# Optimization experiments

Measured on AMD Instinct MI355X. Metric: run time of the kernel, lower is better.

Reference implementation:

```python
import jax, jax.numpy as jnp
import numpy as np

DECAY_MIN = 0.9
DECAY_MAX = 0.999

def setup_inputs() -> dict:
    key = jax.random.key(0)
    ks = jax.random.split(key, 6)
    B, L, D, M = 8, 4096, 1024, 64
    s = 0.02
    return {
        "x": jax.random.normal(ks[0], (B, L, D), jnp.float32),
        "Wq": jax.random.normal(ks[1], (D, M), jnp.float32) * s,
        "Wk": jax.random.normal(ks[2], (D, M), jnp.float32) * s,
        "Wv": jax.random.normal(ks[3], (D, M), jnp.float32) * s,
        "Wo": jax.random.normal(ks[4], (M, D), jnp.float32) * s,
        "bo": jnp.zeros((D,), jnp.float32),
        "Wg": jax.random.normal(ks[5], (D, 1), jnp.float32) * s,
        "bg": jnp.zeros((1,), jnp.float32),
        "decay_param": jnp.full((1,), 0.5, jnp.float32),
    }

def reference(x, Wq, Wk, Wv, Wo, bo, Wg, bg, decay_param):
    B, L, D = x.shape
    M = Wq.shape[1]
    # decay in [DECAY_MIN, DECAY_MAX], shape (1,) -> scalar broadcast
    decay = DECAY_MIN + jax.nn.sigmoid(decay_param) * (DECAY_MAX - DECAY_MIN)
    q = x @ Wq  # (B,L,M)
    k = x @ Wk
    v = x @ Wv
    gates = jax.nn.sigmoid(x @ Wg + bg)[..., 0]  # (B,L)
    S0 = jnp.zeros((B, M, M), x.dtype)

    def scan_fn(S, inp):
        q_t, k_t, v_t, g_t = inp  # (B,M),(B,M),(B,M),(B,)
        gk = k_t * g_t[:, None]
        gv = v_t * g_t[:, None]
        # fast-weight update: S = decay*S + gk ⊗ gv
        S = decay * S + gk[:, :, None] * gv[:, None, :]
        out_t = jnp.einsum('bd,bde->be', q_t, S)
        return S, out_t

    S_final, outs = jax.lax.scan(
        scan_fn, S0,
        (q.transpose(1, 0, 2), k.transpose(1, 0, 2), v.transpose(1, 0, 2), gates.T))
    outs = outs.transpose(1, 0, 2)  # (B,L,M)
    y = outs @ Wo + bo  # (B,L,D); dropout deterministic (eval)
    return y, S_final
```

## Files before the change

kernel.cpp:

```cpp
#include <hip/hip_runtime.h>
#include <math.h>

#define B_SZ 8
#define L_SZ 4096
#define D_SZ 1024
#define M_SZ 64
#define ROWS (B_SZ * L_SZ)
#define NCHUNK 64
#define CHUNK 64

#define FMA4(acc, sc, v) { (acc).x += (sc)*(v).x; (acc).y += (sc)*(v).y; (acc).z += (sc)*(v).z; (acc).w += (sc)*(v).w; }
#define SCALE4(v, sc) { (v).x *= (sc); (v).y *= (sc); (v).z *= (sc); (v).w *= (sc); }

typedef __attribute__((ext_vector_type(8))) short bf16x8;
typedef __attribute__((ext_vector_type(4))) float f32x4;

__device__ __forceinline__ float sigmoid_f(float z) { return 1.0f / (1.0f + __expf(-z)); }
__device__ __forceinline__ float decay_of(const float* __restrict__ dp) {
  return 0.9f + (0.999f - 0.9f) * sigmoid_f(dp[0]);
}
__device__ __forceinline__ unsigned short f2bf(float f) {
  unsigned int u = __float_as_uint(f);
  unsigned int r = (u + 0x7FFFu + ((u >> 16) & 1u)) >> 16;
  return (unsigned short)r;
}

__device__ __forceinline__ void gl2lds16(const void* g, void* l) {
  __builtin_amdgcn_global_load_lds(
      (const __attribute__((address_space(1))) unsigned int*)g,
      (__attribute__((address_space(3))) unsigned int*)l, 16, 0, 0);
}

#define BT_CH     1872
#define BT_CH_PAD 1920
#define BT_BYTES  (BT_CH_PAD * 16)
__global__ __launch_bounds__(256) void k0_prep(
    const float* __restrict__ Wq, const float* __restrict__ Wk,
    const float* __restrict__ Wv, const float* __restrict__ Wg,
    unsigned short* __restrict__ Wt)
{
  const int n = blockIdx.x;
  #pragma unroll
  for (int j = 0; j < 5; ++j) {
    int idx = threadIdx.x + 256 * j;
    if (idx < 1152) {
      int kt = idx / 72;
      int r  = idx - kt * 72;
      int c = r >> 3, e = r & 7;
      float v = 0.f;
      if (c < 8 && n < 193) {
        int k = kt * 64 + c * 8 + e;
        v = (n < 64)  ? Wq[(size_t)k * 64 + n]
          : (n < 128) ? Wk[(size_t)k * 64 + (n - 64)]
          : (n < 192) ? Wv[(size_t)k * 64 + (n - 128)]
                      : Wg[k];
      }
      Wt[((size_t)kt * BT_CH_PAD + (size_t)n * 9 + c) * 8 + e] = f2bf(v);
    }
  }
}

#define K1_ROWS 64
#define A_STRIDE 272
#define B_STRIDE 144

__global__ __launch_bounds__(256, 3) void k1_qkvg_mfma(
    const float* __restrict__ x, const unsigned short* __restrict__ Wt,
    const float* __restrict__ bg,
    float* __restrict__ q_ws, float* __restrict__ a_ws, float* __restrict__ b_ws)
{
  __shared__ __align__(16) unsigned char AsB[K1_ROWS * A_STRIDE];
  __shared__ __align__(16) unsigned char BsB[BT_BYTES];

  const int tid  = threadIdx.x;
  const int lane = tid & 63;
  const int w    = tid >> 6;
  const int quad = lane >> 4;
  const int l15  = lane & 15;
  const int row0 = blockIdx.x * K1_ROWS;

  const unsigned char* xb  = (const unsigned char*)(x + (size_t)row0 * D_SZ);
  const unsigned char* wtb = (const unsigned char*)Wt;

  const unsigned char* xA[5];
  #pragma unroll
  for (int i = 0; i < 5; ++i) {
    int ci  = i * 256 + tid;
    int row = ci / 17;
    int c17 = ci - row * 17;
    xA[i] = xb + (size_t)row * 4096 + (c17 < 16 ? c17 * 16 : 0);
  }

  f32x4 acc[13];
  #pragma unroll
  for (int tn = 0; tn < 13; ++tn) acc[tn] = (f32x4){0.f, 0.f, 0.f, 0.f};

  for (int t = 0; t < 16; ++t) {
    #pragma unroll
    for (int i = 0; i < 4; ++i)
      gl2lds16(xA[i] + (size_t)t * 256, AsB + (i * 256 + tid) * 16);
    if (tid < 64)
      gl2lds16(xA[4] + (size_t)t * 256, AsB + (4 * 256 + tid) * 16);
    const unsigned char* wt_t = wtb + (size_t)t * BT_BYTES;
    #pragma unroll
    for (int i = 0; i < 7; ++i)
      gl2lds16(wt_t + (i * 256 + tid) * 16, BsB + (i * 256 + tid) * 16);
    if (tid < 128)
      gl2lds16(wt_t + (7 * 256 + tid) * 16, BsB + (7 * 256 + tid) * 16);

    __syncthreads();

    bf16x8 af[2];
    #pragma unroll
    for (int kt = 0; kt < 2; ++kt) {
      const unsigned char* ap = AsB + (16 * w + l15) * A_STRIDE + kt * 128 + quad * 32;
      float4 lo = *reinterpret_cast<const float4*>(ap);
      float4 hi = *reinterpret_cast<const float4*>(ap + 16);
      uint4 p;
      p.x = (unsigned)f2bf(lo.x) | ((unsigned)f2bf(lo.y) << 16);
      p.y = (unsigned)f2bf(lo.z) | ((unsigned)f2bf(lo.w) << 16);
      p.z = (unsigned)f2bf(hi.x) | ((unsigned)f2bf(hi.y) << 16);
      p.w = (unsigned)f2bf(hi.z) | ((unsigned)f2bf(hi.w) << 16);
      af[kt] = *reinterpret_cast<bf16x8*>(&p);
    }
    #pragma unroll
    for (int tn = 0; tn < 13; ++tn) {
      #pragma unroll
      for (int kt = 0; kt < 2; ++kt) {
        bf16x8 bf = *reinterpret_cast<const bf16x8*>(
            BsB + (tn * 16 + l15) * B_STRIDE + kt * 64 + quad * 16);
        acc[tn] = __builtin_amdgcn_mfma_f32_16x16x32_bf16(af[kt], bf, acc[tn], 0, 0, 0);
      }
    }
    __syncthreads();
  }

  const float bg0 = bg[0];
  float g4[4];
  #pragma unroll
  for (int r = 0; r < 4; ++r) {
    float gv = __shfl(acc[12][r], lane & 48);
    g4[r] = sigmoid_f(gv + bg0);
  }

  float (*T)[68] = (float(*)[68])AsB;
  const int erow = tid >> 2, eq4 = tid & 3;
  #pragma unroll
  for (int p = 0; p < 3; ++p) {
    float* dst = (p == 0) ? q_ws : (p == 1) ? a_ws : b_ws;
    #pragma unroll
    for (int tn4 = 0; tn4 < 4; ++tn4) {
      #pragma unroll
      for (int r = 0; r < 4; ++r) {
        float v = acc[p * 4 + tn4][r];
        if (p > 0) v *= g4[r];
        T[16 * w + quad * 4 + r][tn4 * 16 + l15] = v;
      }
    }
    __syncthreads();
    float4 vv[4];
    #pragma unroll
    for (int j = 0; j < 4; ++j)
      vv[j] = *reinterpret_cast<float4*>(&T[erow][eq4 * 16 + 4 * j]);
    #pragma unroll
    for (int j = 0; j < 4; ++j)
      *reinterpret_cast<float4*>(&dst[(size_t)(row0 + erow) * 64 + eq4 * 16 + 4 * j]) = vv[j];
    if (p < 2) __syncthreads();
  }
}

__global__ __launch_bounds__(256) void k2_delta(
    const float* __restrict__ a_ws, const float* __restrict__ b_ws,
    const float* __restrict__ dp, float* __restrict__ dS)
{
  __shared__ float Aa[64][64];
  __shared__ float Bc[64][64];
  __shared__ float pw[64];
  const int tid = threadIdx.x;
  const int bc = blockIdx.x;
  const int rowbase = (bc >> 6) * L_SZ + (bc & 63) * CHUNK;
  const int s = tid >> 2, m0 = (tid & 3) * 16;
  #pragma unroll
  for (int j = 0; j < 4; ++j) {
    *reinterpret_cast<float4*>(&Aa[s][m0 + 4*j]) =
        *reinterpret_cast<const float4*>(&a_ws[(size_t)(rowbase + s) * 64 + m0 + 4*j]);
    *reinterpret_cast<float4*>(&Bc[s][m0 + 4*j]) =
        *reinterpret_cast<const float4*>(&b_ws[(size_t)(rowbase + s) * 64 + m0 + 4*j]);
  }
  if (tid < 64) pw[tid] = powf(decay_of(dp), (float)(63 - tid));
  __syncthreads();
  const int d0 = tid >> 2, e0 = (tid & 3) * 16;
  float4 o0 = make_float4(0,0,0,0), o1 = o0, o2 = o0, o3 = o0;
  for (int ss = 0; ss < 64; ++ss) {
    float wa = pw[ss] * Aa[ss][d0];
    float4 b0 = *reinterpret_cast<float4*>(&Bc[ss][e0+0]);
    float4 b1 = *reinterpret_cast<float4*>(&Bc[ss][e0+4]);
    float4 b2 = *reinterpret_cast<float4*>(&Bc[ss][e0+8]);
    float4 b3 = *reinterpret_cast<float4*>(&Bc[ss][e0+12]);
    FMA4(o0, wa, b0); FMA4(o1, wa, b1); FMA4(o2, wa, b2); FMA4(o3, wa, b3);
  }
  float* dst = &dS[((size_t)bc << 12) + d0 * 64 + e0];
  *reinterpret_cast<float4*>(dst + 0)  = o0;
  *reinterpret_cast<float4*>(dst + 4)  = o1;
  *reinterpret_cast<float4*>(dst + 8)  = o2;
  *reinterpret_cast<float4*>(dst + 12) = o3;
}

__global__ __launch_bounds__(256) void k3_scan(
    const float* __restrict__ dS, const float* __restrict__ dp,
    float* __restrict__ Sst, float* __restrict__ sfin)
{
  const int g = blockIdx.x * 256 + threadIdx.x;
  const int b = g >> 12;
  const int de = g & 4095;
  const float dC = powf(decay_of(dp), 64.0f);
  const size_t base = ((size_t)(b * 64) << 12) + de;
  float d[NCHUNK];
  #pragma unroll
  for (int c = 0; c < NCHUNK; ++c) d[c] = dS[base + ((size_t)c << 12)];
  float s = 0.f;
  #pragma unroll
  for (int c = 0; c < NCHUNK; ++c) {
    Sst[base + ((size_t)c << 12)] = s;
    s = dC * s + d[c];
  }
  sfin[((size_t)b << 12) + de] = s;
}

__global__ __launch_bounds__(256) void k4_intra(
    const float* __restrict__ q_ws, const float* __restrict__ a_ws,
    const float* __restrict__ b_ws, const float* __restrict__ Sst,
    const float* __restrict__ dp, float* __restrict__ outs)
{
  __shared__ float Qs[64][68];
  __shared__ float Ps[64][68];
  __shared__ float Bs[64][64];
  __shared__ float S0s[64][64];
  __shared__ float pw[65];
  const int tid = threadIdx.x;
  const int bc = blockIdx.x;
  const int rowbase = (bc >> 6) * L_SZ + (bc & 63) * CHUNK;
  const int s = tid >> 2, m0 = (tid & 3) * 16;
  #pragma unroll
  for (int j = 0; j < 4; ++j) {
    float4 qv = *reinterpret_cast<const float4*>(&q_ws[(size_t)(rowbase + s) * 64 + m0 + 4*j]);
    Qs[s][m0+4*j+0] = qv.x; Qs[s][m0+4*j+1] = qv.y; Qs[s][m0+4*j+2] = qv.z; Qs[s][m0+4*j+3] = qv.w;
    float4 av = *reinterpret_cast<const float4*>(&a_ws[(size_t)(rowbase + s) * 64 + m0 + 4*j]);
    Ps[m0+4*j+0][s] = av.x; Ps[m0+4*j+1][s] = av.y; Ps[m0+4*j+2][s] = av.z; Ps[m0+4*j+3][s] = av.w;
    float4 bv = *reinterpret_cast<const float4*>(&b_ws[(size_t)(rowbase + s) * 64 + m0 + 4*j]);
    *reinterpret_cast<float4*>(&Bs[s][m0+4*j]) = bv;
    float4 sv = *reinterpret_cast<const float4*>(&Sst[((size_t)bc << 12) + tid*16 + 4*j]);
    *reinterpret_cast<float4*>(&(&S0s[0][0])[tid*16 + 4*j]) = sv;
  }
  if (tid < 65) pw[tid] = powf(decay_of(dp), (float)tid);
  __syncthreads();

  const int t0 = tid >> 2, c0 = (tid & 3) * 16;
  float4 r0 = make_float4(0,0,0,0), r1 = r0, r2 = r0, r3 = r0;
  for (int m = 0; m < 64; ++m) {
    float qv = Qs[t0][m];
    float4 a0 = *reinterpret_cast<float4*>(&Ps[m][c0+0]);
    float4 a1 = *reinterpret_cast<float4*>(&Ps[m][c0+4]);
    float4 a2 = *reinterpret_cast<float4*>(&Ps[m][c0+8]);
    float4 a3 = *reinterpret_cast<float4*>(&Ps[m][c0+12]);
    FMA4(r0, qv, a0); FMA4(r1, qv, a1); FMA4(r2, qv, a2); FMA4(r3, qv, a3);
  }
  float rr[16] = {r0.x,r0.y,r0.z,r0.w, r1.x,r1.y,r1.z,r1.w,
                  r2.x,r2.y,r2.z,r2.w, r3.x,r3.y,r3.z,r3.w};
  __syncthreads();
  #pragma unroll
  for (int j = 0; j < 16; ++j) {
    const int sidx = c0 + j;
    Ps[t0][sidx] = (sidx <= t0) ? rr[j] * pw[t0 - sidx] : 0.f;
  }
  __syncthreads();

  float4 o0 = make_float4(0,0,0,0), o1 = o0, o2 = o0, o3 = o0;
  for (int m = 0; m < 64; ++m) {
    float qv = Qs[t0][m];
    float4 v0 = *reinterpret_cast<float4*>(&S0s[m][c0+0]);
    float4 v1 = *reinterpret_cast<float4*>(&S0s[m][c0+4]);
    float4 v2 = *reinterpret_cast<float4*>(&S0s[m][c0+8]);
    float4 v3 = *reinterpret_cast<float4*>(&S0s[m][c0+12]);
    FMA4(o0, qv, v0); FMA4(o1, qv, v1); FMA4(o2, qv, v2); FMA4(o3, qv, v3);
  }
  const float dsc = pw[t0 + 1];
  SCALE4(o0, dsc); SCALE4(o1, dsc); SCALE4(o2, dsc); SCALE4(o3, dsc);
  for (int ss = 0; ss < 64; ++ss) {
    float pv = Ps[t0][ss];
    float4 b0 = *reinterpret_cast<float4*>(&Bs[ss][c0+0]);
    float4 b1 = *reinterpret_cast<float4*>(&Bs[ss][c0+4]);
    float4 b2 = *reinterpret_cast<float4*>(&Bs[ss][c0+8]);
    float4 b3 = *reinterpret_cast<float4*>(&Bs[ss][c0+12]);
    FMA4(o0, pv, b0); FMA4(o1, pv, b1); FMA4(o2, pv, b2); FMA4(o3, pv, b3);
  }
  float* dst = &outs[(size_t)(rowbase + t0) * 64 + c0];
  *reinterpret_cast<float4*>(dst + 0)  = o0;
  *reinterpret_cast<float4*>(dst + 4)  = o1;
  *reinterpret_cast<float4*>(dst + 8)  = o2;
  *reinterpret_cast<float4*>(dst + 12) = o3;
}

__global__ __launch_bounds__(256) void k5_proj(
    const float* __restrict__ outs, const float* __restrict__ Wo,
    const float* __restrict__ bo, float* __restrict__ y)
{
  __shared__ float Os[64][65];
  __shared__ float Ws[64][64];
  const int tid = threadIdx.x;
  const int tx = tid & 15, ty = tid >> 4;
  const int row0 = blockIdx.x * 64;
  const int n0 = blockIdx.y * 64;
  const int s = tid >> 2, m0 = (tid & 3) * 16;
  #pragma unroll
  for (int j = 0; j < 4; ++j) {
    float4 ov = *reinterpret_cast<const float4*>(&outs[(size_t)(row0 + s) * 64 + m0 + 4*j]);
    Os[s][m0+4*j+0] = ov.x; Os[s][m0+4*j+1] = ov.y; Os[s][m0+4*j+2] = ov.z; Os[s][m0+4*j+3] = ov.w;
    float4 wv = *reinterpret_cast<const float4*>(&Wo[(size_t)s * D_SZ + n0 + m0 + 4*j]);
    *reinterpret_cast<float4*>(&Ws[s][m0+4*j]) = wv;
  }
  __syncthreads();
  float4 acc[4];
  #pragma unroll
  for (int r = 0; r < 4; ++r) acc[r] = make_float4(0,0,0,0);
  for (int kk = 0; kk < 64; ++kk) {
    float a0 = Os[4*ty+0][kk];
    float a1 = Os[4*ty+1][kk];
    float a2 = Os[4*ty+2][kk];
    float a3 = Os[4*ty+3][kk];
    float4 w = *reinterpret_cast<float4*>(&Ws[kk][4*tx]);
    FMA4(acc[0], a0, w); FMA4(acc[1], a1, w); FMA4(acc[2], a2, w); FMA4(acc[3], a3, w);
  }
  float4 bv = *reinterpret_cast<const float4*>(&bo[n0 + 4*tx]);
  #pragma unroll
  for (int r = 0; r < 4; ++r) {
    float4 res;
    res.x = acc[r].x + bv.x; res.y = acc[r].y + bv.y;
    res.z = acc[r].z + bv.z; res.w = acc[r].w + bv.w;
    *reinterpret_cast<float4*>(&y[(size_t)(row0 + 4*ty + r) * D_SZ + n0 + 4*tx]) = res;
  }
}

extern "C" void kernel_launch(void* const* d_in, const int* in_sizes, int n_in,
                              void* d_out, int out_size, void* d_ws, size_t ws_size,
                              hipStream_t stream) {
  (void)in_sizes; (void)n_in; (void)out_size; (void)ws_size;
  const float* x  = (const float*)d_in[0];
  const float* Wq = (const float*)d_in[1];
  const float* Wk = (const float*)d_in[2];
  const float* Wv = (const float*)d_in[3];
  const float* Wo = (const float*)d_in[4];
  const float* bo = (const float*)d_in[5];
  const float* Wg = (const float*)d_in[6];
  const float* bg = (const float*)d_in[7];
  const float* dp = (const float*)d_in[8];

  float* y    = (float*)d_out;
  float* sfin = y + (size_t)B_SZ * L_SZ * D_SZ;

  float* ws   = (float*)d_ws;
  const size_t SEG = (size_t)ROWS * M_SZ;
  float* q_ws = ws;
  float* a_ws = q_ws + SEG;
  float* b_ws = a_ws + SEG;
  float* dS   = b_ws + SEG;
  float* Sst  = dS   + SEG;
  float* outs = Sst  + SEG;
  unsigned short* Wt = (unsigned short*)outs;

  k0_prep<<<dim3(208), dim3(256), 0, stream>>>(Wq, Wk, Wv, Wg, Wt);
  k1_qkvg_mfma<<<dim3(ROWS / K1_ROWS), dim3(256), 0, stream>>>(x, Wt, bg, q_ws, a_ws, b_ws);
  k2_delta<<<dim3(B_SZ * NCHUNK), dim3(256), 0, stream>>>(a_ws, b_ws, dp, dS);
  k3_scan<<<dim3((B_SZ * M_SZ * M_SZ) / 256), dim3(256), 0, stream>>>(dS, dp, Sst, sfin);
  k4_intra<<<dim3(B_SZ * NCHUNK), dim3(256), 0, stream>>>(q_ws, a_ws, b_ws, Sst, dp, outs);
  k5_proj<<<dim3(ROWS / 64, D_SZ / 64), dim3(256), 0, stream>>>(outs, Wo, bo, y);
}
```

Measured before the change: 358.5 us.

## Move output projection onto bf16 MFMA with split-precision hi/lo operands

Replaces the scalar FP32 output projection with an MFMA kernel. A new prep kernel splits Wo into bf16 high and low parts in a transposed, padded layout, and the activation tile is split the same way in shared memory. Three bf16 products (hh, lh, hl) approximate FP32 accuracy. Results are staged through LDS so the y stores are coalesced. This targets the compute cost of the final 32768x1024x64 GEMM, which also has a large output write, at the price of an extra prep launch and roughly 3x MFMA work per product.

```diff
diff --git a/kernel.cpp b/kernel.cpp
--- a/kernel.cpp
+++ b/kernel.cpp
@@ -60,6 +60,33 @@
   }
 }
 
+__global__ __launch_bounds__(256) void k0b_wo(
+    const float* __restrict__ Wo, unsigned short* __restrict__ woth,
+    unsigned short* __restrict__ wotl)
+{
+  const int n = blockIdx.x * 256 + threadIdx.x;
+  unsigned int hp[36], lp[36];
+  #pragma unroll
+  for (int kp = 0; kp < 32; ++kp) {
+    float v0 = Wo[(size_t)(2 * kp) * D_SZ + n];
+    float v1 = Wo[(size_t)(2 * kp + 1) * D_SZ + n];
+    unsigned short h0 = f2bf(v0), h1 = f2bf(v1);
+    unsigned short l0 = f2bf(v0 - __uint_as_float((unsigned)h0 << 16));
+    unsigned short l1 = f2bf(v1 - __uint_as_float((unsigned)h1 << 16));
+    hp[kp] = (unsigned)h0 | ((unsigned)h1 << 16);
+    lp[kp] = (unsigned)l0 | ((unsigned)l1 << 16);
+  }
+  #pragma unroll
+  for (int kp = 32; kp < 36; ++kp) { hp[kp] = 0; lp[kp] = 0; }
+  #pragma unroll
+  for (int j = 0; j < 9; ++j) {
+    uint4 uh = make_uint4(hp[4*j], hp[4*j+1], hp[4*j+2], hp[4*j+3]);
+    uint4 ul = make_uint4(lp[4*j], lp[4*j+1], lp[4*j+2], lp[4*j+3]);
+    *reinterpret_cast<uint4*>(&woth[(size_t)n * 72 + 8 * j]) = uh;
+    *reinterpret_cast<uint4*>(&wotl[(size_t)n * 72 + 8 * j]) = ul;
+  }
+}
+
 #define K1_ROWS 64
 #define A_STRIDE 272
 #define B_STRIDE 144
@@ -301,43 +328,101 @@
   *reinterpret_cast<float4*>(dst + 12) = o3;
 }
 
-__global__ __launch_bounds__(256) void k5_proj(
-    const float* __restrict__ outs, const float* __restrict__ Wo,
-    const float* __restrict__ bo, float* __restrict__ y)
-{
-  __shared__ float Os[64][65];
-  __shared__ float Ws[64][64];
-  const int tid = threadIdx.x;
-  const int tx = tid & 15, ty = tid >> 4;
+#define K5_CB 128
+__global__ __launch_bounds__(256, 2) void k5_mfma(
+    const float* __restrict__ outs, const unsigned short* __restrict__ woth,
+    const unsigned short* __restrict__ wotl, const float* __restrict__ bo,
+    float* __restrict__ y)
+{
+  __shared__ __align__(16) unsigned char L[55296];
+  unsigned short* Ah = (unsigned short*)L;
+  unsigned short* Al = Ah + 64 * 72;
+  unsigned short* Bh = Al + 64 * 72;
+  unsigned short* Bl = Bh + 128 * 72;
+  float* T = (float*)L;
+
+  const int tid  = threadIdx.x;
+  const int lane = tid & 63;
+  const int w    = tid >> 6;
+  const int quad = lane >> 4;
+  const int l15  = lane & 15;
   const int row0 = blockIdx.x * 64;
-  const int n0 = blockIdx.y * 64;
-  const int s = tid >> 2, m0 = (tid & 3) * 16;
-  #pragma unroll
-  for (int j = 0; j < 4; ++j) {
-    float4 ov = *reinterpret_cast<const float4*>(&outs[(size_t)(row0 + s) * 64 + m0 + 4*j]);
-    Os[s][m0+4*j+0] = ov.x; Os[s][m0+4*j+1] = ov.y; Os[s][m0+4*j+2] = ov.z; Os[s][m0+4*j+3] = ov.w;
-    float4 wv = *reinterpret_cast<const float4*>(&Wo[(size_t)s * D_SZ + n0 + m0 + 4*j]);
-    *reinterpret_cast<float4*>(&Ws[s][m0+4*j]) = wv;
-  }
-  __syncthreads();
-  float4 acc[4];
-  #pragma unroll
-  for (int r = 0; r < 4; ++r) acc[r] = make_float4(0,0,0,0);
-  for (int kk = 0; kk < 64; ++kk) {
-    float a0 = Os[4*ty+0][kk];
-    float a1 = Os[4*ty+1][kk];
-    float a2 = Os[4*ty+2][kk];
-    float a3 = Os[4*ty+3][kk];
-    float4 w = *reinterpret_cast<float4*>(&Ws[kk][4*tx]);
-    FMA4(acc[0], a0, w); FMA4(acc[1], a1, w); FMA4(acc[2], a2, w); FMA4(acc[3], a3, w);
-  }
-  float4 bv = *reinterpret_cast<const float4*>(&bo[n0 + 4*tx]);
-  #pragma unroll
-  for (int r = 0; r < 4; ++r) {
-    float4 res;
-    res.x = acc[r].x + bv.x; res.y = acc[r].y + bv.y;
-    res.z = acc[r].z + bv.z; res.w = acc[r].w + bv.w;
-    *reinterpret_cast<float4*>(&y[(size_t)(row0 + 4*ty + r) * D_SZ + n0 + 4*tx]) = res;
+  const int n0   = blockIdx.y * K5_CB;
+
+  const unsigned char* bsh = (const unsigned char*)(woth + (size_t)n0 * 72);
+  const unsigned char* bsl = (const unsigned char*)(wotl + (size_t)n0 * 72);
+  #pragma unroll
+  for (int i = 0; i < 4; ++i) {
+    gl2lds16(bsh + (i * 256 + tid) * 16, (unsigned char*)Bh + (i * 256 + tid) * 16);
+    gl2lds16(bsl + (i * 256 + tid) * 16, (unsigned char*)Bl + (i * 256 + tid) * 16);
+  }
+  if (tid < 128) {
+    gl2lds16(bsh + (1024 + tid) * 16, (unsigned char*)Bh + (1024 + tid) * 16);
+    gl2lds16(bsl + (1024 + tid) * 16, (unsigned char*)Bl + (1024 + tid) * 16);
+  }
+
+  {
+    const int ar = tid >> 2, kc = (tid & 3) * 16;
+    float av[16];
+    #pragma unroll
+    for (int j = 0; j < 4; ++j) {
+      float4 v = *reinterpret_cast<const float4*>(&outs[(size_t)(row0 + ar) * 64 + kc + 4 * j]);
+      av[4*j+0] = v.x; av[4*j+1] = v.y; av[4*j+2] = v.z; av[4*j+3] = v.w;
+    }
+    unsigned int hp[8], lp[8];
+    #pragma unroll
+    for (int e = 0; e < 8; ++e) {
+      unsigned short h0 = f2bf(av[2*e]), h1 = f2bf(av[2*e+1]);
+      unsigned short l0 = f2bf(av[2*e]   - __uint_as_float((unsigned)h0 << 16));
+      unsigned short l1 = f2bf(av[2*e+1] - __uint_as_float((unsigned)h1 << 16));
+      hp[e] = (unsigned)h0 | ((unsigned)h1 << 16);
+      lp[e] = (unsigned)l0 | ((unsigned)l1 << 16);
+    }
+    *reinterpret_cast<uint4*>(&Ah[ar*72 + kc])     = make_uint4(hp[0],hp[1],hp[2],hp[3]);
+    *reinterpret_cast<uint4*>(&Ah[ar*72 + kc + 8]) = make_uint4(hp[4],hp[5],hp[6],hp[7]);
+    *reinterpret_cast<uint4*>(&Al[ar*72 + kc])     = make_uint4(lp[0],lp[1],lp[2],lp[3]);
+    *reinterpret_cast<uint4*>(&Al[ar*72 + kc + 8]) = make_uint4(lp[4],lp[5],lp[6],lp[7]);
+  }
+  __syncthreads();
+
+  bf16x8 afh[2], afl[2];
+  #pragma unroll
+  for (int kt = 0; kt < 2; ++kt) {
+    afh[kt] = *reinterpret_cast<bf16x8*>(&Ah[(16*w + l15)*72 + kt*32 + quad*8]);
+    afl[kt] = *reinterpret_cast<bf16x8*>(&Al[(16*w + l15)*72 + kt*32 + quad*8]);
+  }
+  f32x4 acc[8];
+  #pragma unroll
+  for (int cf = 0; cf < 8; ++cf) acc[cf] = (f32x4){0.f, 0.f, 0.f, 0.f};
+  #pragma unroll
+  for (int cf = 0; cf < 8; ++cf) {
+    bf16x8 bh0 = *reinterpret_cast<bf16x8*>(&Bh[(cf*16 + l15)*72 + quad*8]);
+    bf16x8 bh1 = *reinterpret_cast<bf16x8*>(&Bh[(cf*16 + l15)*72 + 32 + quad*8]);
+    bf16x8 bl0 = *reinterpret_cast<bf16x8*>(&Bl[(cf*16 + l15)*72 + quad*8]);
+    bf16x8 bl1 = *reinterpret_cast<bf16x8*>(&Bl[(cf*16 + l15)*72 + 32 + quad*8]);
+    acc[cf] = __builtin_amdgcn_mfma_f32_16x16x32_bf16(afh[0], bh0, acc[cf], 0, 0, 0);
+    acc[cf] = __builtin_amdgcn_mfma_f32_16x16x32_bf16(afh[1], bh1, acc[cf], 0, 0, 0);
+    acc[cf] = __builtin_amdgcn_mfma_f32_16x16x32_bf16(afl[0], bh0, acc[cf], 0, 0, 0);
+    acc[cf] = __builtin_amdgcn_mfma_f32_16x16x32_bf16(afl[1], bh1, acc[cf], 0, 0, 0);
+    acc[cf] = __builtin_amdgcn_mfma_f32_16x16x32_bf16(afh[0], bl0, acc[cf], 0, 0, 0);
+    acc[cf] = __builtin_amdgcn_mfma_f32_16x16x32_bf16(afh[1], bl1, acc[cf], 0, 0, 0);
+  }
+  __syncthreads();
+
+  #pragma unroll
+  for (int cf = 0; cf < 8; ++cf)
+    #pragma unroll
+    for (int r = 0; r < 4; ++r)
+      T[(16*w + quad*4 + r) * 132 + cf*16 + l15] = acc[cf][r];
+  __syncthreads();
+
+  const int er = tid >> 2, ec = (tid & 3) * 32;
+  #pragma unroll
+  for (int j = 0; j < 8; ++j) {
+    float4 v = *reinterpret_cast<float4*>(&T[er*132 + ec + 4*j]);
+    float4 b = *reinterpret_cast<const float4*>(&bo[n0 + ec + 4*j]);
+    v.x += b.x; v.y += b.y; v.z += b.z; v.w += b.w;
+    *reinterpret_cast<float4*>(&y[(size_t)(row0 + er) * D_SZ + n0 + ec + 4*j]) = v;
   }
 }
 
@@ -367,11 +452,14 @@
   float* Sst  = dS   + SEG;
   float* outs = Sst  + SEG;
   unsigned short* Wt = (unsigned short*)outs;
+  unsigned short* woth = (unsigned short*)(outs + SEG);
+  unsigned short* wotl = woth + (size_t)1024 * 72;
 
   k0_prep<<<dim3(208), dim3(256), 0, stream>>>(Wq, Wk, Wv, Wg, Wt);
+  k0b_wo<<<dim3(4), dim3(256), 0, stream>>>(Wo, woth, wotl);
   k1_qkvg_mfma<<<dim3(ROWS / K1_ROWS), dim3(256), 0, stream>>>(x, Wt, bg, q_ws, a_ws, b_ws);
   k2_delta<<<dim3(B_SZ * NCHUNK), dim3(256), 0, stream>>>(a_ws, b_ws, dp, dS);
   k3_scan<<<dim3((B_SZ * M_SZ * M_SZ) / 256), dim3(256), 0, stream>>>(dS, dp, Sst, sfin);
   k4_intra<<<dim3(B_SZ * NCHUNK), dim3(256), 0, stream>>>(q_ws, a_ws, b_ws, Sst, dp, outs);
-  k5_proj<<<dim3(ROWS / 64, D_SZ / 64), dim3(256), 0, stream>>>(outs, Wo, bo, y);
-}
+  k5_mfma<<<dim3(ROWS / 64, D_SZ / K5_CB), dim3(256), 0, stream>>>(outs, woth, wotl, bo, y);
+}
```

New measurement: 370.7 us. +3.4%, slower.

## Double-buffer x tiles with XOR-swizzled LDS in the QKVG projection GEMM

Applied to the files above, without the earlier changes.

The projection kernel now stages x tiles into two LDS buffers, prefetching tile t+1 while computing tile t. It uses a partial vmcnt wait with raw s_barrier instead of two full __syncthreads per iteration. The padded A layout is replaced by an XOR swizzle to avoid LDS bank conflicts, and the weight tile is padded to 2048 chunks so every thread loads uniformly. In exchange, LDS use grows and the occupancy hint drops from 3 to 2 blocks per CU, which may reduce latency hiding.

```diff
diff --git a/kernel.cpp b/kernel.cpp
--- a/kernel.cpp
+++ b/kernel.cpp
@@ -31,8 +31,7 @@
       (__attribute__((address_space(3))) unsigned int*)l, 16, 0, 0);
 }
 
-#define BT_CH     1872
-#define BT_CH_PAD 1920
+#define BT_CH_PAD 2048
 #define BT_BYTES  (BT_CH_PAD * 16)
 __global__ __launch_bounds__(256) void k0_prep(
     const float* __restrict__ Wq, const float* __restrict__ Wk,
@@ -61,16 +60,15 @@
 }
 
 #define K1_ROWS 64
-#define A_STRIDE 272
 #define B_STRIDE 144
 
-__global__ __launch_bounds__(256, 3) void k1_qkvg_mfma(
+__global__ __launch_bounds__(256, 2) void k1_qkvg_mfma(
     const float* __restrict__ x, const unsigned short* __restrict__ Wt,
     const float* __restrict__ bg,
     float* __restrict__ q_ws, float* __restrict__ a_ws, float* __restrict__ b_ws)
 {
-  __shared__ __align__(16) unsigned char AsB[K1_ROWS * A_STRIDE];
-  __shared__ __align__(16) unsigned char BsB[BT_BYTES];
+  __shared__ __align__(16) unsigned char As[2][16384];
+  __shared__ __align__(16) unsigned char Bs[BT_BYTES];
 
   const int tid  = threadIdx.x;
   const int lane = tid & 63;
@@ -82,40 +80,39 @@
   const unsigned char* xb  = (const unsigned char*)(x + (size_t)row0 * D_SZ);
   const unsigned char* wtb = (const unsigned char*)Wt;
 
-  const unsigned char* xA[5];
-  #pragma unroll
-  for (int i = 0; i < 5; ++i) {
-    int ci  = i * 256 + tid;
-    int row = ci / 17;
-    int c17 = ci - row * 17;
-    xA[i] = xb + (size_t)row * 4096 + (c17 < 16 ? c17 * 16 : 0);
+  const unsigned char* xAsrc[4];
+  #pragma unroll
+  for (int i = 0; i < 4; ++i) {
+    int c   = i * 256 + tid;
+    int row = c >> 4, c16 = c & 15;
+    xAsrc[i] = xb + (size_t)row * 4096 + ((c16 * 16) ^ ((row & 7) << 4));
   }
 
   f32x4 acc[13];
   #pragma unroll
   for (int tn = 0; tn < 13; ++tn) acc[tn] = (f32x4){0.f, 0.f, 0.f, 0.f};
 
-  for (int t = 0; t < 16; ++t) {
+  const int arow = 16 * w + l15;
+  const int sw   = (l15 & 7) << 4;
+
+  auto stageA = [&](int buf, int t) {
     #pragma unroll
     for (int i = 0; i < 4; ++i)
-      gl2lds16(xA[i] + (size_t)t * 256, AsB + (i * 256 + tid) * 16);
-    if (tid < 64)
-      gl2lds16(xA[4] + (size_t)t * 256, AsB + (4 * 256 + tid) * 16);
+      gl2lds16(xAsrc[i] + (size_t)t * 256, As[buf] + (i * 256 + tid) * 16);
+  };
+  auto stageB = [&](int t) {
     const unsigned char* wt_t = wtb + (size_t)t * BT_BYTES;
     #pragma unroll
-    for (int i = 0; i < 7; ++i)
-      gl2lds16(wt_t + (i * 256 + tid) * 16, BsB + (i * 256 + tid) * 16);
-    if (tid < 128)
-      gl2lds16(wt_t + (7 * 256 + tid) * 16, BsB + (7 * 256 + tid) * 16);
-
-    __syncthreads();
-
+    for (int i = 0; i < 8; ++i)
+      gl2lds16(wt_t + (i * 256 + tid) * 16, Bs + (i * 256 + tid) * 16);
+  };
+  auto compute = [&](int buf) {
     bf16x8 af[2];
+    const unsigned char* ap = As[buf] + arow * 256;
     #pragma unroll
     for (int kt = 0; kt < 2; ++kt) {
-      const unsigned char* ap = AsB + (16 * w + l15) * A_STRIDE + kt * 128 + quad * 32;
-      float4 lo = *reinterpret_cast<const float4*>(ap);
-      float4 hi = *reinterpret_cast<const float4*>(ap + 16);
+      float4 lo = *reinterpret_cast<const float4*>(ap + ((kt * 128 + quad * 32) ^ sw));
+      float4 hi = *reinterpret_cast<const float4*>(ap + ((kt * 128 + quad * 32 + 16) ^ sw));
       uint4 p;
       p.x = (unsigned)f2bf(lo.x) | ((unsigned)f2bf(lo.y) << 16);
       p.y = (unsigned)f2bf(lo.z) | ((unsigned)f2bf(lo.w) << 16);
@@ -128,12 +125,31 @@
       #pragma unroll
       for (int kt = 0; kt < 2; ++kt) {
         bf16x8 bf = *reinterpret_cast<const bf16x8*>(
-            BsB + (tn * 16 + l15) * B_STRIDE + kt * 64 + quad * 16);
+            Bs + (tn * 16 + l15) * B_STRIDE + kt * 64 + quad * 16);
         acc[tn] = __builtin_amdgcn_mfma_f32_16x16x32_bf16(af[kt], bf, acc[tn], 0, 0, 0);
       }
     }
-    __syncthreads();
-  }
+  };
+
+  stageA(0, 0);
+  for (int t = 0; t < 15; ++t) {
+    const int cur = t & 1;
+    stageB(t);
+    stageA(cur ^ 1, t + 1);
+    asm volatile("s_waitcnt vmcnt(4)" ::: "memory");
+    __builtin_amdgcn_sched_barrier(0);
+    __builtin_amdgcn_s_barrier();
+    compute(cur);
+    asm volatile("s_waitcnt lgkmcnt(0)" ::: "memory");
+    __builtin_amdgcn_sched_barrier(0);
+    __builtin_amdgcn_s_barrier();
+  }
+  stageB(15);
+  asm volatile("s_waitcnt vmcnt(0)" ::: "memory");
+  __builtin_amdgcn_sched_barrier(0);
+  __builtin_amdgcn_s_barrier();
+  compute(1);
+  __syncthreads();
 
   const float bg0 = bg[0];
   float g4[4];
@@ -143,7 +159,7 @@
     g4[r] = sigmoid_f(gv + bg0);
   }
 
-  float (*T)[68] = (float(*)[68])AsB;
+  float (*T)[68] = (float(*)[68])As;
   const int erow = tid >> 2, eq4 = tid & 3;
   #pragma unroll
   for (int p = 0; p < 3; ++p) {
```

Result: no change. 352.3 us (-1.7%).
